# Kernel tuning notes

Hardware: AMD Instinct MI355X
Metric: run time of the kernel (lower is better)

Reference implementation:

```python
import jax, jax.numpy as jnp
import numpy as np

N_NODES = 2048
N_EDGES = 32768
D_IN = 128      # input_dimension
D_MEM_H = 128   # mem_hidden_dimension
D_MEM_A = 128   # mem_agg_hidden_dimension
D_AGG_H = 128   # agg_hidden_dimension
D_OUT = 128     # output_dimension
D_FEAT = 32     # feature_dimension


def setup_inputs() -> dict:
    key = jax.random.key(0)
    ks = jax.random.split(key, 10)
    state = jax.random.normal(ks[0], (N_EDGES, D_IN), dtype=jnp.float32)
    feature = jax.random.normal(ks[1], (N_EDGES, D_FEAT), dtype=jnp.float32)
    mask = (jax.random.uniform(ks[2], (N_NODES, N_EDGES)) < 0.005).astype(jnp.float32)
    mask_transpose = mask.T
    s = 0.05
    W1_m = jax.random.normal(ks[3], (D_MEM_H, D_IN), dtype=jnp.float32) * s
    b1_m = jax.random.normal(ks[4], (D_MEM_H,), dtype=jnp.float32) * s
    W2_m = jax.random.normal(ks[5], (D_MEM_A, D_MEM_H), dtype=jnp.float32) * s
    W1_a = jax.random.normal(ks[6], (D_AGG_H, D_MEM_A + D_FEAT), dtype=jnp.float32) * s
    b1_a = jax.random.normal(ks[7], (D_AGG_H,), dtype=jnp.float32) * s
    W2_a = jax.random.normal(ks[8], (D_OUT, D_AGG_H), dtype=jnp.float32) * s
    return {"state": state, "feature": feature, "mask": mask,
            "mask_transpose": mask_transpose,
            "W1_m": W1_m, "b1_m": b1_m, "W2_m": W2_m,
            "W1_a": W1_a, "b1_a": b1_a, "W2_a": W2_a}


def reference(state, feature, mask, mask_transpose, W1_m, b1_m, W2_m, W1_a, b1_a, W2_a):
    ls = jax.nn.log_sigmoid
    # memory MLP: [E, D_IN] -> [E, D_MEM_A]
    s = ls(ls(state @ W1_m.T + b1_m) @ W2_m.T)
    # bipartite aggregation: gather per-node sums, scatter back to edges
    agg = mask_transpose @ (mask @ s) - s  # include_self_message=False
    # concat features and aggregation MLP: [E, D_MEM_A + D_FEAT] -> [E, D_OUT]
    agg = jnp.concatenate((agg, feature), axis=1)
    out = ls(ls(agg @ W1_a.T + b1_a) @ W2_a.T)
    return out
```

## Files before the change

kernel.cpp:

```cpp
#include <hip/hip_runtime.h>
#include <cstdint>
#include <cstddef>

#define N_NODES 2048
#define N_EDGES 32768
#define ROW_CAP 384
#define COL_CAP 48

typedef unsigned short u16;
typedef __bf16 bf16x8 __attribute__((ext_vector_type(8)));
typedef float f32x4 __attribute__((ext_vector_type(4)));
typedef uint32_t u32x4 __attribute__((ext_vector_type(4)));

union BF8 {
  bf16x8 v;
  u16 s[8];
  uint4 q;
};

__device__ __forceinline__ u16 f2bf(float f) {
  uint32_t u = __float_as_uint(f);
  uint32_t r = (u + 0x7fffu + ((u >> 16) & 1u)) >> 16;
  return (u16)r;
}
__device__ __forceinline__ float bf2f(u16 h) {
  return __uint_as_float(((uint32_t)h) << 16);
}
__device__ __forceinline__ float logsig(float x) {
  return fminf(x, 0.0f) - __logf(1.0f + __expf(-fabsf(x)));
}

__device__ __forceinline__ BF8 load_f32x8_bf(const float* __restrict__ p) {
  const float4 g0 = ((const float4*)p)[0];
  const float4 g1 = ((const float4*)p)[1];
  BF8 b;
  b.s[0] = f2bf(g0.x); b.s[1] = f2bf(g0.y);
  b.s[2] = f2bf(g0.z); b.s[3] = f2bf(g0.w);
  b.s[4] = f2bf(g1.x); b.s[5] = f2bf(g1.y);
  b.s[6] = f2bf(g1.z); b.s[7] = f2bf(g1.w);
  return b;
}

__global__ __launch_bounds__(256) void mlp_m(
    const float* __restrict__ state, const float* __restrict__ W1m,
    const float* __restrict__ b1, const float* __restrict__ W2m,
    u16* __restrict__ s_out, int* __restrict__ col_cnt)
{
  const int tid = threadIdx.x;
  const int gi = blockIdx.x * 256 + tid;
  if (gi < N_EDGES) col_cnt[gi] = 0;

  const int wave = tid >> 6;
  const int lane = tid & 63;
  const int l16 = lane & 15;
  const int quad = lane >> 4;
  const int row0 = blockIdx.x * 128;

  __shared__ u16 h_lds[128][136];

  const f32x4 vzero = {0.f, 0.f, 0.f, 0.f};
  f32x4 acc[2][8];
  for (int rt = 0; rt < 2; ++rt)
    for (int ct = 0; ct < 8; ++ct) acc[rt][ct] = vzero;

  for (int kc = 0; kc < 4; ++kc) {
    const int k0 = kc * 32 + quad * 8;
    BF8 a[2];
    for (int rt = 0; rt < 2; ++rt)
      a[rt] = load_f32x8_bf(state + (size_t)(row0 + wave * 32 + rt * 16 + l16) * 128 + k0);
    for (int ct = 0; ct < 8; ++ct) {
      const BF8 b = load_f32x8_bf(W1m + (size_t)(ct * 16 + l16) * 128 + k0);
      for (int rt = 0; rt < 2; ++rt)
        acc[rt][ct] = __builtin_amdgcn_mfma_f32_16x16x32_bf16(a[rt].v, b.v, acc[rt][ct], 0, 0, 0);
    }
  }

  for (int ct = 0; ct < 8; ++ct) {
    const int col = ct * 16 + l16;
    const float bias = b1[col];
    for (int rt = 0; rt < 2; ++rt) {
      const int r = wave * 32 + rt * 16 + quad * 4;
      for (int i = 0; i < 4; ++i)
        h_lds[r + i][col] = f2bf(logsig(acc[rt][ct][i] + bias));
    }
  }
  __syncthreads();

  f32x4 acc2[2][8];
  for (int rt = 0; rt < 2; ++rt)
    for (int ct = 0; ct < 8; ++ct) acc2[rt][ct] = vzero;

  for (int kc = 0; kc < 4; ++kc) {
    const int k0 = kc * 32 + quad * 8;
    BF8 a[2];
    for (int rt = 0; rt < 2; ++rt)
      a[rt].q = *(const uint4*)&h_lds[wave * 32 + rt * 16 + l16][k0];
    for (int ct = 0; ct < 8; ++ct) {
      const BF8 b = load_f32x8_bf(W2m + (size_t)(ct * 16 + l16) * 128 + k0);
      for (int rt = 0; rt < 2; ++rt)
        acc2[rt][ct] = __builtin_amdgcn_mfma_f32_16x16x32_bf16(a[rt].v, b.v, acc2[rt][ct], 0, 0, 0);
    }
  }

  for (int ct = 0; ct < 8; ++ct) {
    const int col = ct * 16 + l16;
    for (int rt = 0; rt < 2; ++rt) {
      const int r = row0 + wave * 32 + rt * 16 + quad * 4;
      for (int i = 0; i < 4; ++i)
        s_out[(size_t)(r + i) * 128 + col] = f2bf(logsig(acc2[rt][ct][i]));
    }
  }
}

__global__ __launch_bounds__(256) void scan_gather(
    const float* __restrict__ mask, const u16* __restrict__ s_bf,
    int* __restrict__ col_cnt, int* __restrict__ col_nodes,
    float* __restrict__ y)
{
  const int n = blockIdx.x;
  const int tid = threadIdx.x;
  const int lane = tid & 63;

  __shared__ int cnt;
  __shared__ int list[ROW_CAP];
  __shared__ float part[3][128];

  if (tid == 0) cnt = 0;
  __syncthreads();

  const u32x4* row = (const u32x4*)(mask + (size_t)n * N_EDGES);
  u32x4 v0 = __builtin_nontemporal_load(&row[tid]);
  u32x4 v1 = __builtin_nontemporal_load(&row[tid + 256]);
#pragma unroll 1
  for (int t = 0; t < 16; ++t) {
    const int i = tid + t * 512;
    u32x4 n0 = {0u, 0u, 0u, 0u}, n1 = {0u, 0u, 0u, 0u};
    if (t < 15) {
      n0 = __builtin_nontemporal_load(&row[i + 512]);
      n1 = __builtin_nontemporal_load(&row[i + 768]);
    }
#pragma unroll
    for (int h = 0; h < 2; ++h) {
      const u32x4 v = h ? v1 : v0;
      const int ib = i + h * 256;
      const uint32_t any = v[0] | v[1] | v[2] | v[3];
      const unsigned long long many = __ballot(any != 0u);
      if (many) {
#pragma unroll
        for (int k = 0; k < 4; ++k) {
          const bool p = (v[k] != 0u);
          const unsigned long long m = __ballot(p);
          if (m) {
            int base = 0;
            if (lane == 0) base = atomicAdd(&cnt, __popcll(m));
            base = __shfl(base, 0);
            if (p) {
              const int off = __popcll(m & ((1ull << lane) - 1ull));
              if (base + off < ROW_CAP) list[base + off] = ib * 4 + k;
            }
          }
        }
      }
    }
    v0 = n0; v1 = n1;
  }
  __syncthreads();

  const int c = min(cnt, ROW_CAP);

  for (int i = tid; i < c; i += 256) {
    const int e = list[i];
    const int slot = atomicAdd(&col_cnt[e], 1);
    if (slot < COL_CAP) col_nodes[(size_t)e * COL_CAP + slot] = n;
  }

  const int wv = tid >> 6;
  const int d0 = lane * 2;
  float a0 = 0.f, a1 = 0.f;
#pragma unroll 4
  for (int i = wv; i < c; i += 4) {
    const uint32_t sp = *(const uint32_t*)&s_bf[(size_t)list[i] * 128 + d0];
    a0 += bf2f((u16)(sp & 0xffffu));
    a1 += bf2f((u16)(sp >> 16));
  }
  if (wv > 0) { part[wv - 1][d0] = a0; part[wv - 1][d0 + 1] = a1; }
  __syncthreads();
  if (wv == 0) {
    a0 += part[0][d0] + part[1][d0] + part[2][d0];
    a1 += part[0][d0 + 1] + part[1][d0 + 1] + part[2][d0 + 1];
    float2 r; r.x = a0; r.y = a1;
    *(float2*)&y[n * 128 + d0] = r;
  }
}

__global__ __launch_bounds__(256) void pass_b(
    const float* __restrict__ y, const u16* __restrict__ s_bf,
    const float* __restrict__ feature, const int* __restrict__ col_cnt,
    const int* __restrict__ col_nodes, u16* __restrict__ cat)
{
  const int lane = threadIdx.x & 63;
  const int e = blockIdx.x * 4 + (threadIdx.x >> 6);
  const int d0 = lane * 2;
  const int cnt = min(col_cnt[e], COL_CAP);
  const int cnl = col_nodes[(size_t)e * COL_CAP + min(lane, COL_CAP - 1)];
  float a0 = 0.f, a1 = 0.f;
#pragma unroll 4
  for (int j = 0; j < cnt; ++j) {
    const int nn = __shfl(cnl, j);
    const float2 yv = *(const float2*)&y[nn * 128 + d0];
    a0 += yv.x; a1 += yv.y;
  }
  const uint32_t sp = *(const uint32_t*)&s_bf[(size_t)e * 128 + d0];
  a0 -= bf2f((u16)(sp & 0xffffu));
  a1 -= bf2f((u16)(sp >> 16));
  const uint32_t packed = (uint32_t)f2bf(a0) | ((uint32_t)f2bf(a1) << 16);
  *(uint32_t*)&cat[(size_t)e * 160 + d0] = packed;
  if (lane < 16) {
    const float2 fv = *(const float2*)&feature[e * 32 + lane * 2];
    const uint32_t pf = (uint32_t)f2bf(fv.x) | ((uint32_t)f2bf(fv.y) << 16);
    *(uint32_t*)&cat[(size_t)e * 160 + 128 + lane * 2] = pf;
  }
}

__global__ __launch_bounds__(256) void mlp_a_kernel(
    const u16* __restrict__ cat, const float* __restrict__ W1a,
    const float* __restrict__ b1, const float* __restrict__ W2a,
    float* __restrict__ out)
{
  const int tid = threadIdx.x;
  const int wave = tid >> 6;
  const int lane = tid & 63;
  const int l16 = lane & 15;
  const int quad = lane >> 4;
  const int row0 = blockIdx.x * 128;

  __shared__ u16 h_lds[128][136];

  const f32x4 vzero = {0.f, 0.f, 0.f, 0.f};
  f32x4 acc[2][8];
  for (int rt = 0; rt < 2; ++rt)
    for (int ct = 0; ct < 8; ++ct) acc[rt][ct] = vzero;

  for (int kc = 0; kc < 5; ++kc) {
    const int k0 = kc * 32 + quad * 8;
    BF8 a[2];
    for (int rt = 0; rt < 2; ++rt)
      a[rt].q = *(const uint4*)(cat + (size_t)(row0 + wave * 32 + rt * 16 + l16) * 160 + k0);
    for (int ct = 0; ct < 8; ++ct) {
      const BF8 b = load_f32x8_bf(W1a + (size_t)(ct * 16 + l16) * 160 + k0);
      for (int rt = 0; rt < 2; ++rt)
        acc[rt][ct] = __builtin_amdgcn_mfma_f32_16x16x32_bf16(a[rt].v, b.v, acc[rt][ct], 0, 0, 0);
    }
  }

  for (int ct = 0; ct < 8; ++ct) {
    const int col = ct * 16 + l16;
    const float bias = b1[col];
    for (int rt = 0; rt < 2; ++rt) {
      const int r = wave * 32 + rt * 16 + quad * 4;
      for (int i = 0; i < 4; ++i)
        h_lds[r + i][col] = f2bf(logsig(acc[rt][ct][i] + bias));
    }
  }
  __syncthreads();

  f32x4 acc2[2][8];
  for (int rt = 0; rt < 2; ++rt)
    for (int ct = 0; ct < 8; ++ct) acc2[rt][ct] = vzero;

  for (int kc = 0; kc < 4; ++kc) {
    const int k0 = kc * 32 + quad * 8;
    BF8 a[2];
    for (int rt = 0; rt < 2; ++rt)
      a[rt].q = *(const uint4*)&h_lds[wave * 32 + rt * 16 + l16][k0];
    for (int ct = 0; ct < 8; ++ct) {
      const BF8 b = load_f32x8_bf(W2a + (size_t)(ct * 16 + l16) * 128 + k0);
      for (int rt = 0; rt < 2; ++rt)
        acc2[rt][ct] = __builtin_amdgcn_mfma_f32_16x16x32_bf16(a[rt].v, b.v, acc2[rt][ct], 0, 0, 0);
    }
  }

  for (int ct = 0; ct < 8; ++ct) {
    const int col = ct * 16 + l16;
    for (int rt = 0; rt < 2; ++rt) {
      const int r = row0 + wave * 32 + rt * 16 + quad * 4;
      for (int i = 0; i < 4; ++i)
        out[(size_t)(r + i) * 128 + col] = logsig(acc2[rt][ct][i]);
    }
  }
}

extern "C" void kernel_launch(void* const* d_in, const int* in_sizes, int n_in,
                              void* d_out, int out_size, void* d_ws, size_t ws_size,
                              hipStream_t stream)
{
  const float* state   = (const float*)d_in[0];
  const float* feature = (const float*)d_in[1];
  const float* mask    = (const float*)d_in[2];
  const float* W1m = (const float*)d_in[4];
  const float* b1m = (const float*)d_in[5];
  const float* W2m = (const float*)d_in[6];
  const float* W1a = (const float*)d_in[7];
  const float* b1a = (const float*)d_in[8];
  const float* W2a = (const float*)d_in[9];
  float* out = (float*)d_out;

  char* ws = (char*)d_ws;
  u16*  s_bf      = (u16*)(ws);
  u16*  cat       = (u16*)(ws + 8388608);
  float* y        = (float*)(ws + 18874368);
  int*  col_cnt   = (int*)(ws + 19922944);
  int*  col_nodes = (int*)(ws + 20054016);

  mlp_m<<<256, 256, 0, stream>>>(state, W1m, b1m, W2m, s_bf, col_cnt);
  scan_gather<<<N_NODES, 256, 0, stream>>>(mask, s_bf, col_cnt, col_nodes, y);
  pass_b<<<N_EDGES / 4, 256, 0, stream>>>(y, s_bf, feature, col_cnt, col_nodes, cat);
  mlp_a_kernel<<<N_EDGES / 128, 256, 0, stream>>>(cat, W1a, b1a, W2a, out);
}
```

Measured before the change: 594.3 us.

## Preconvert weights to bf16 once and halve MLP tile rows per block

Result: faster. 537.2 us (-9.6%).

```diff
diff --git a/kernel.cpp b/kernel.cpp
--- a/kernel.cpp
+++ b/kernel.cpp
@@ -41,74 +41,75 @@
   return b;
 }
 
+__global__ __launch_bounds__(256) void conv_weights(
+    const float* __restrict__ W1m, const float* __restrict__ W2m,
+    const float* __restrict__ W1a, const float* __restrict__ W2a,
+    u16* __restrict__ wb, int* __restrict__ col_cnt)
+{
+  const int i = blockIdx.x * 256 + threadIdx.x;
+  if (i < N_EDGES) col_cnt[i] = 0;
+  if (i < 16384)      wb[i] = f2bf(W1m[i]);
+  else if (i < 32768) wb[i] = f2bf(W2m[i - 16384]);
+  else if (i < 53248) wb[i] = f2bf(W1a[i - 32768]);
+  else if (i < 69632) wb[i] = f2bf(W2a[i - 53248]);
+}
+
 __global__ __launch_bounds__(256) void mlp_m(
-    const float* __restrict__ state, const float* __restrict__ W1m,
-    const float* __restrict__ b1, const float* __restrict__ W2m,
-    u16* __restrict__ s_out, int* __restrict__ col_cnt)
+    const float* __restrict__ state, const u16* __restrict__ W1b,
+    const float* __restrict__ b1, const u16* __restrict__ W2b,
+    u16* __restrict__ s_out)
 {
   const int tid = threadIdx.x;
-  const int gi = blockIdx.x * 256 + tid;
-  if (gi < N_EDGES) col_cnt[gi] = 0;
-
   const int wave = tid >> 6;
   const int lane = tid & 63;
   const int l16 = lane & 15;
   const int quad = lane >> 4;
-  const int row0 = blockIdx.x * 128;
-
-  __shared__ u16 h_lds[128][136];
+  const int row0 = blockIdx.x * 64;
+
+  __shared__ u16 h_lds[64][136];
 
   const f32x4 vzero = {0.f, 0.f, 0.f, 0.f};
-  f32x4 acc[2][8];
-  for (int rt = 0; rt < 2; ++rt)
-    for (int ct = 0; ct < 8; ++ct) acc[rt][ct] = vzero;
+  f32x4 acc[8];
+  for (int ct = 0; ct < 8; ++ct) acc[ct] = vzero;
 
   for (int kc = 0; kc < 4; ++kc) {
     const int k0 = kc * 32 + quad * 8;
-    BF8 a[2];
-    for (int rt = 0; rt < 2; ++rt)
-      a[rt] = load_f32x8_bf(state + (size_t)(row0 + wave * 32 + rt * 16 + l16) * 128 + k0);
+    const BF8 a = load_f32x8_bf(state + (size_t)(row0 + wave * 16 + l16) * 128 + k0);
     for (int ct = 0; ct < 8; ++ct) {
-      const BF8 b = load_f32x8_bf(W1m + (size_t)(ct * 16 + l16) * 128 + k0);
-      for (int rt = 0; rt < 2; ++rt)
-        acc[rt][ct] = __builtin_amdgcn_mfma_f32_16x16x32_bf16(a[rt].v, b.v, acc[rt][ct], 0, 0, 0);
+      BF8 b;
+      b.q = *(const uint4*)(W1b + (size_t)(ct * 16 + l16) * 128 + k0);
+      acc[ct] = __builtin_amdgcn_mfma_f32_16x16x32_bf16(a.v, b.v, acc[ct], 0, 0, 0);
     }
   }
 
   for (int ct = 0; ct < 8; ++ct) {
     const int col = ct * 16 + l16;
     const float bias = b1[col];
-    for (int rt = 0; rt < 2; ++rt) {
-      const int r = wave * 32 + rt * 16 + quad * 4;
-      for (int i = 0; i < 4; ++i)
-        h_lds[r + i][col] = f2bf(logsig(acc[rt][ct][i] + bias));
-    }
-  }
-  __syncthreads();
-
-  f32x4 acc2[2][8];
-  for (int rt = 0; rt < 2; ++rt)
-    for (int ct = 0; ct < 8; ++ct) acc2[rt][ct] = vzero;
+    const int r = wave * 16 + quad * 4;
+    for (int i = 0; i < 4; ++i)
+      h_lds[r + i][col] = f2bf(logsig(acc[ct][i] + bias));
+  }
+  __syncthreads();
+
+  f32x4 acc2[8];
+  for (int ct = 0; ct < 8; ++ct) acc2[ct] = vzero;
 
   for (int kc = 0; kc < 4; ++kc) {
     const int k0 = kc * 32 + quad * 8;
-    BF8 a[2];
-    for (int rt = 0; rt < 2; ++rt)
-      a[rt].q = *(const uint4*)&h_lds[wave * 32 + rt * 16 + l16][k0];
+    BF8 a;
+    a.q = *(const uint4*)&h_lds[wave * 16 + l16][k0];
     for (int ct = 0; ct < 8; ++ct) {
-      const BF8 b = load_f32x8_bf(W2m + (size_t)(ct * 16 + l16) * 128 + k0);
-      for (int rt = 0; rt < 2; ++rt)
-        acc2[rt][ct] = __builtin_amdgcn_mfma_f32_16x16x32_bf16(a[rt].v, b.v, acc2[rt][ct], 0, 0, 0);
+      BF8 b;
+      b.q = *(const uint4*)(W2b + (size_t)(ct * 16 + l16) * 128 + k0);
+      acc2[ct] = __builtin_amdgcn_mfma_f32_16x16x32_bf16(a.v, b.v, acc2[ct], 0, 0, 0);
     }
   }
 
   for (int ct = 0; ct < 8; ++ct) {
     const int col = ct * 16 + l16;
-    for (int rt = 0; rt < 2; ++rt) {
-      const int r = row0 + wave * 32 + rt * 16 + quad * 4;
-      for (int i = 0; i < 4; ++i)
-        s_out[(size_t)(r + i) * 128 + col] = f2bf(logsig(acc2[rt][ct][i]));
-    }
+    const int r = row0 + wave * 16 + quad * 4;
+    for (int i = 0; i < 4; ++i)
+      s_out[(size_t)(r + i) * 128 + col] = f2bf(logsig(acc2[ct][i]));
   }
 }
 
@@ -203,6 +204,9 @@
   const int d0 = lane * 2;
   const int cnt = min(col_cnt[e], COL_CAP);
   const int cnl = col_nodes[(size_t)e * COL_CAP + min(lane, COL_CAP - 1)];
+  const uint32_t sp = *(const uint32_t*)&s_bf[(size_t)e * 128 + d0];
+  float2 fv = {0.f, 0.f};
+  if (lane < 16) fv = *(const float2*)&feature[e * 32 + lane * 2];
   float a0 = 0.f, a1 = 0.f;
 #pragma unroll 4
   for (int j = 0; j < cnt; ++j) {
@@ -210,21 +214,19 @@
     const float2 yv = *(const float2*)&y[nn * 128 + d0];
     a0 += yv.x; a1 += yv.y;
   }
-  const uint32_t sp = *(const uint32_t*)&s_bf[(size_t)e * 128 + d0];
   a0 -= bf2f((u16)(sp & 0xffffu));
   a1 -= bf2f((u16)(sp >> 16));
   const uint32_t packed = (uint32_t)f2bf(a0) | ((uint32_t)f2bf(a1) << 16);
   *(uint32_t*)&cat[(size_t)e * 160 + d0] = packed;
   if (lane < 16) {
-    const float2 fv = *(const float2*)&feature[e * 32 + lane * 2];
     const uint32_t pf = (uint32_t)f2bf(fv.x) | ((uint32_t)f2bf(fv.y) << 16);
     *(uint32_t*)&cat[(size_t)e * 160 + 128 + lane * 2] = pf;
   }
 }
 
 __global__ __launch_bounds__(256) void mlp_a_kernel(
-    const u16* __restrict__ cat, const float* __restrict__ W1a,
-    const float* __restrict__ b1, const float* __restrict__ W2a,
+    const u16* __restrict__ cat, const u16* __restrict__ W1b,
+    const float* __restrict__ b1, const u16* __restrict__ W2b,
     float* __restrict__ out)
 {
   const int tid = threadIdx.x;
@@ -232,61 +234,53 @@
   const int lane = tid & 63;
   const int l16 = lane & 15;
   const int quad = lane >> 4;
-  const int row0 = blockIdx.x * 128;
-
-  __shared__ u16 h_lds[128][136];
+  const int row0 = blockIdx.x * 64;
+
+  __shared__ u16 h_lds[64][136];
 
   const f32x4 vzero = {0.f, 0.f, 0.f, 0.f};
-  f32x4 acc[2][8];
-  for (int rt = 0; rt < 2; ++rt)
-    for (int ct = 0; ct < 8; ++ct) acc[rt][ct] = vzero;
+  f32x4 acc[8];
+  for (int ct = 0; ct < 8; ++ct) acc[ct] = vzero;
 
   for (int kc = 0; kc < 5; ++kc) {
     const int k0 = kc * 32 + quad * 8;
-    BF8 a[2];
-    for (int rt = 0; rt < 2; ++rt)
-      a[rt].q = *(const uint4*)(cat + (size_t)(row0 + wave * 32 + rt * 16 + l16) * 160 + k0);
+    BF8 a;
+    a.q = *(const uint4*)(cat + (size_t)(row0 + wave * 16 + l16) * 160 + k0);
     for (int ct = 0; ct < 8; ++ct) {
-      const BF8 b = load_f32x8_bf(W1a + (size_t)(ct * 16 + l16) * 160 + k0);
-      for (int rt = 0; rt < 2; ++rt)
-        acc[rt][ct] = __builtin_amdgcn_mfma_f32_16x16x32_bf16(a[rt].v, b.v, acc[rt][ct], 0, 0, 0);
+      BF8 b;
+      b.q = *(const uint4*)(W1b + (size_t)(ct * 16 + l16) * 160 + k0);
+      acc[ct] = __builtin_amdgcn_mfma_f32_16x16x32_bf16(a.v, b.v, acc[ct], 0, 0, 0);
     }
   }
 
   for (int ct = 0; ct < 8; ++ct) {
     const int col = ct * 16 + l16;
     const float bias = b1[col];
-    for (int rt = 0; rt < 2; ++rt) {
-      const int r = wave * 32 + rt * 16 + quad * 4;
-      for (int i = 0; i < 4; ++i)
-        h_lds[r + i][col] = f2bf(logsig(acc[rt][ct][i] + bias));
-    }
-  }
-  __syncthreads();
-
-  f32x4 acc2[2][8];
-  for (int rt = 0; rt < 2; ++rt)
-    for (int ct = 0; ct < 8; ++ct) acc2[rt][ct] = vzero;
+    const int r = wave * 16 + quad * 4;
+    for (int i = 0; i < 4; ++i)
+      h_lds[r + i][col] = f2bf(logsig(acc[ct][i] + bias));
+  }
+  __syncthreads();
+
+  f32x4 acc2[8];
+  for (int ct = 0; ct < 8; ++ct) acc2[ct] = vzero;
 
   for (int kc = 0; kc < 4; ++kc) {
     const int k0 = kc * 32 + quad * 8;
-    BF8 a[2];
-    for (int rt = 0; rt < 2; ++rt)
-      a[rt].q = *(const uint4*)&h_lds[wave * 32 + rt * 16 + l16][k0];
+    BF8 a;
+    a.q = *(const uint4*)&h_lds[wave * 16 + l16][k0];
     for (int ct = 0; ct < 8; ++ct) {
-      const BF8 b = load_f32x8_bf(W2a + (size_t)(ct * 16 + l16) * 128 + k0);
-      for (int rt = 0; rt < 2; ++rt)
-        acc2[rt][ct] = __builtin_amdgcn_mfma_f32_16x16x32_bf16(a[rt].v, b.v, acc2[rt][ct], 0, 0, 0);
+      BF8 b;
+      b.q = *(const uint4*)(W2b + (size_t)(ct * 16 + l16) * 128 + k0);
+      acc2[ct] = __builtin_amdgcn_mfma_f32_16x16x32_bf16(a.v, b.v, acc2[ct], 0, 0, 0);
     }
   }
 
   for (int ct = 0; ct < 8; ++ct) {
     const int col = ct * 16 + l16;
-    for (int rt = 0; rt < 2; ++rt) {
-      const int r = row0 + wave * 32 + rt * 16 + quad * 4;
-      for (int i = 0; i < 4; ++i)
-        out[(size_t)(r + i) * 128 + col] = logsig(acc2[rt][ct][i]);
-    }
+    const int r = row0 + wave * 16 + quad * 4;
+    for (int i = 0; i < 4; ++i)
+      out[(size_t)(r + i) * 128 + col] = logsig(acc2[ct][i]);
   }
 }
 
@@ -311,9 +305,11 @@
   float* y        = (float*)(ws + 18874368);
   int*  col_cnt   = (int*)(ws + 19922944);
   int*  col_nodes = (int*)(ws + 20054016);
-
-  mlp_m<<<256, 256, 0, stream>>>(state, W1m, b1m, W2m, s_bf, col_cnt);
+  u16*  wb        = (u16*)(ws + 26345472);
+
+  conv_weights<<<272, 256, 0, stream>>>(W1m, W2m, W1a, W2a, wb, col_cnt);
+  mlp_m<<<512, 256, 0, stream>>>(state, wb, b1m, wb + 16384, s_bf);
   scan_gather<<<N_NODES, 256, 0, stream>>>(mask, s_bf, col_cnt, col_nodes, y);
   pass_b<<<N_EDGES / 4, 256, 0, stream>>>(y, s_bf, feature, col_cnt, col_nodes, cat);
-  mlp_a_kernel<<<N_EDGES / 128, 256, 0, stream>>>(cat, W1a, b1a, W2a, out);
-}
+  mlp_a_kernel<<<512, 256, 0, stream>>>(cat, wb + 32768, b1a, wb + 53248, out);
+}
```
